# Optimization experiments

Measured on AMD Instinct MI355X. Metric: run time of the kernel, lower is better.

## Reference

```python
import jax, jax.numpy as jnp
import numpy as np

V_IPC, N_ROLES, D = 50000, 16, 256
B, L = 2048, 64
F_BIB, H1, H2, D_OUT = 512, 1024, 1024, 512
N_EXP, N_CLS = 8, 10
LN_EPS = 1e-5


def setup_inputs() -> dict:
    key = jax.random.key(0)
    ks = jax.random.split(key, 24)
    s = 0.05
    ipc_emb = jax.random.normal(ks[0], (V_IPC, D), jnp.float32) * s
    ipc_emb = ipc_emb.at[0].set(0.0)  # padding_idx=0
    role_emb = jax.random.normal(ks[1], (N_ROLES, D), jnp.float32) * s
    role_emb = role_emb.at[0].set(0.0)
    inp = {
        "ipc_indices": jax.random.randint(ks[2], (B, L), 0, V_IPC),
        "role_indices": jax.random.randint(ks[3], (B, L), 0, N_ROLES),
        "bibliometric_features": jax.random.normal(ks[4], (B, F_BIB), jnp.float32),
        "ipc_padding_mask": jax.random.randint(ks[5], (B, L), 0, 2).astype(jnp.int32),
        "top_k": 2,
        "ipc_emb": ipc_emb,
        "role_emb": role_emb,
        "Wq": jax.random.normal(ks[6], (D, D), jnp.float32) * s,
        "bq": jnp.zeros((D,), jnp.float32),
        "Wk": jax.random.normal(ks[7], (D, D), jnp.float32) * s,
        "bk": jnp.zeros((D,), jnp.float32),
        "Wv": jax.random.normal(ks[8], (D, D), jnp.float32) * s,
        "bv": jnp.zeros((D,), jnp.float32),
        "global_context": jax.random.normal(ks[9], (D,), jnp.float32) * s,
        "ln_g": jnp.ones((D,), jnp.float32),
        "ln_b": jnp.zeros((D,), jnp.float32),
        "gate_W": jax.random.normal(ks[10], (D, N_EXP), jnp.float32) * s,
        "gate_b": jnp.zeros((N_EXP,), jnp.float32),
        "expert_biases": jnp.zeros((N_EXP,), jnp.float32),
        "W1": jax.random.normal(ks[11], (N_EXP, F_BIB, H1), jnp.float32) * s,
        "b1": jnp.zeros((N_EXP, H1), jnp.float32),
        "W2": jax.random.normal(ks[12], (N_EXP, H1, H2), jnp.float32) * s,
        "b2": jnp.zeros((N_EXP, H2), jnp.float32),
        "W3": jax.random.normal(ks[13], (N_EXP, H2, D_OUT), jnp.float32) * s,
        "b3": jnp.zeros((N_EXP, D_OUT), jnp.float32),
        "head_W": jax.random.normal(ks[14], (D_OUT, N_CLS), jnp.float32) * s,
        "head_b": jnp.zeros((N_CLS,), jnp.float32),
    }
    return inp


def reference(ipc_indices, role_indices, bibliometric_features, ipc_padding_mask, top_k,
              ipc_emb, role_emb, Wq, bq, Wk, bk, Wv, bv, global_context, ln_g, ln_b,
              gate_W, gate_b, expert_biases, W1, b1, W2, b2, W3, b3, head_W, head_b):
    # embeddings + role combine  -> [B, L, D]
    x = ipc_emb[ipc_indices] + role_emb[role_indices]
    # attention pooling with a global learned query (same query for every batch row)
    keys = x @ Wk + bk                                  # [B, L, D]
    values = x @ Wv + bv                                # [B, L, D]
    q = global_context @ Wq + bq                        # [D]
    scores = jnp.einsum('d,bld->bl', q, keys)           # [B, L]
    scores = jnp.where(ipc_padding_mask == 0, -1e9, scores)
    attn = jax.nn.softmax(scores, axis=-1)              # [B, L]
    pooled = jnp.einsum('bl,bld->bd', attn, values)     # [B, D]
    mu = pooled.mean(-1, keepdims=True)
    var = ((pooled - mu) ** 2).mean(-1, keepdims=True)
    router_in = (pooled - mu) / jnp.sqrt(var + LN_EPS) * ln_g + ln_b
    # router: select with biased scores, gate with unbiased scores
    affinity = router_in @ gate_W + gate_b              # [B, E]
    sel_scores = affinity + expert_biases
    _, idx = jax.lax.top_k(sel_scores, top_k)           # [B, K]
    gw = jax.nn.softmax(jnp.take_along_axis(affinity, idx, axis=-1), axis=-1)  # [B, K]
    # dense all-expert MLP (reference form of masked per-expert loop)
    h = jax.nn.relu(jnp.einsum('bi,eih->ebh', bibliometric_features, W1) + b1[:, None, :])
    h = jax.nn.relu(jnp.einsum('ebh,ehj->ebj', h, W2) + b2[:, None, :])
    eo = jnp.einsum('ebj,ejo->ebo', h, W3) + b3[:, None, :]  # [E, B, O]
    # gather each token's top-k expert outputs and combine
    bidx = jnp.arange(idx.shape[0])[:, None]            # [B, 1]
    sel_out = eo[idx, bidx]                             # [B, K, O]
    moe_out = jnp.einsum('bk,bko->bo', gw, sel_out)     # [B, O]
    logits = moe_out @ head_W + head_b                  # [B, n_classes]
    return logits, idx
```

## Files before the change

kernel.cpp:

```cpp
#include <hip/hip_runtime.h>
#include <hip/hip_bf16.h>
#include <math.h>


#define LN_EPS 1e-5f

typedef __bf16 bf16_t;
typedef __bf16 bf16x8 __attribute__((ext_vector_type(8)));
typedef float f32x4 __attribute__((ext_vector_type(4)));

struct f4x2 { float4 a, b; };
__device__ __forceinline__ f4x2 ldA8(const float* p) {
  f4x2 v; v.a = *(const float4*)p; v.b = *(const float4*)(p + 4); return v;
}
__device__ __forceinline__ bf16x8 cvt8(const f4x2& v) {
  bf16x8 o;
  o[0] = (bf16_t)v.a.x; o[1] = (bf16_t)v.a.y; o[2] = (bf16_t)v.a.z; o[3] = (bf16_t)v.a.w;
  o[4] = (bf16_t)v.b.x; o[5] = (bf16_t)v.b.y; o[6] = (bf16_t)v.b.z; o[7] = (bf16_t)v.b.w;
  return o;
}

__global__ __launch_bounds__(256)
void prep_kq_kernel(const float* __restrict__ Wq, const float* __restrict__ bq,
                    const float* __restrict__ Wk, const float* __restrict__ bk,
                    const float* __restrict__ gc, float* __restrict__ kq_out,
                    int* __restrict__ done_ctr) {
  __shared__ float q[256];
  __shared__ float red[4];
  const int t = threadIdx.x, bi = blockIdx.x;
  if (bi == 0 && t == 0) *done_ctr = 0;
  float s = bq[t];
  for (int d = 0; d < 256; d++) s += gc[d] * Wq[d * 256 + t];
  q[t] = s;
  __syncthreads();
  const int rl = t >> 5, sl = t & 31;
  const int r = bi * 8 + rl;
  float p = 0.f;
#pragma unroll
  for (int i = 0; i < 8; i++) { const int d = sl + 32 * i; p += Wk[r * 256 + d] * q[d]; }
#pragma unroll
  for (int o = 16; o > 0; o >>= 1) p += __shfl_down(p, o, 32);
  if (sl == 0) kq_out[r] = p;
  if (bi == 0) {
    float z2 = q[t] * bk[t];
    const int lane = t & 63, wave = t >> 6;
#pragma unroll
    for (int o = 32; o > 0; o >>= 1) z2 += __shfl_down(z2, o);
    if (lane == 0) red[wave] = z2;
    __syncthreads();
    if (t == 0) kq_out[256] = red[0] + red[1] + red[2] + red[3];
  }
}

__global__ __launch_bounds__(256)
void xbar_transpose(const float* __restrict__ W1, const float* __restrict__ W2,
                    const float* __restrict__ W3, bf16_t* __restrict__ B1,
                    bf16_t* __restrict__ B2, bf16_t* __restrict__ B3h,
                    float* __restrict__ b3h_g,
                    const float* __restrict__ b3, const float* __restrict__ head_W,
                    const int* __restrict__ ipc_idx, const int* __restrict__ role_idx,
                    const int* __restrict__ maskp,
                    const float* __restrict__ ipc_emb, const float* __restrict__ role_emb,
                    const float* __restrict__ kq_qbk, float* __restrict__ xbar_g) {
  __shared__ __align__(16) float smem[4480];
  const int bid = blockIdx.x;
  const int t = threadIdx.x, lane = t & 63;

  if (bid < 2048) {
    const int b = bid, wave = t >> 6;
    float* sred = smem;
    float* scores_s = smem + 4352;
    float* attn_s = smem + 4416;
    const float4 kq = *(const float4*)(kq_qbk + lane * 4);
    const float qbk = kq_qbk[256];
    const int rbase = b * 64 + wave * 16;
    int4 m4[4], i4[4], r4[4];
#pragma unroll
    for (int j = 0; j < 4; j++) {
      m4[j] = *(const int4*)(maskp + rbase + j * 4);
      i4[j] = *(const int4*)(ipc_idx + rbase + j * 4);
      r4[j] = *(const int4*)(role_idx + rbase + j * 4);
    }
#pragma unroll
    for (int i = 0; i < 16; i++) {
      const int mki = (&m4[i / 4].x)[i % 4];
      const int ii = mki ? (&i4[i / 4].x)[i % 4] : 0;
      const int ri = mki ? (&r4[i / 4].x)[i % 4] : 0;
      const float4 xe = *(const float4*)(ipc_emb + (size_t)ii * 256 + lane * 4);
      const float4 re = *(const float4*)(role_emb + (size_t)ri * 256 + lane * 4);
      sred[(wave * 64 + lane) * 17 + i] =
          (xe.x + re.x) * kq.x + (xe.y + re.y) * kq.y +
          (xe.z + re.z) * kq.z + (xe.w + re.w) * kq.w;
    }
    __syncthreads();
    {
      const int i_r = lane & 15, g = lane >> 4;
      float s = 0.f;
#pragma unroll
      for (int j = 0; j < 16; j++) s += sred[(wave * 64 + g * 16 + j) * 17 + i_r];
      s += __shfl_xor(s, 16);
      s += __shfl_xor(s, 32);
      const int mval = (&m4[i_r / 4].x)[i_r % 4];
      if (lane < 16) scores_s[wave * 16 + lane] = mval ? (s + qbk) : -1e9f;
    }
    __syncthreads();
    if (wave == 0) {
      const float sv = scores_s[lane];
      float m = sv;
#pragma unroll
      for (int o = 32; o > 0; o >>= 1) m = fmaxf(m, __shfl_xor(m, o));
      const float ev = expf(sv - m);
      float sum = ev;
#pragma unroll
      for (int o = 32; o > 0; o >>= 1) sum += __shfl_xor(sum, o);
      attn_s[lane] = ev / sum;
    }
    __syncthreads();
    float p0 = 0.f, p1 = 0.f, p2 = 0.f, p3 = 0.f;
#pragma unroll
    for (int i = 0; i < 16; i++) {
      const int mki = (&m4[i / 4].x)[i % 4];
      const int ii = mki ? (&i4[i / 4].x)[i % 4] : 0;
      const int ri = mki ? (&r4[i / 4].x)[i % 4] : 0;
      const float a = attn_s[wave * 16 + i];
      const float4 xe = *(const float4*)(ipc_emb + (size_t)ii * 256 + lane * 4);
      const float4 re = *(const float4*)(role_emb + (size_t)ri * 256 + lane * 4);
      p0 += a * (xe.x + re.x); p1 += a * (xe.y + re.y);
      p2 += a * (xe.z + re.z); p3 += a * (xe.w + re.w);
    }
    __syncthreads();
    *(float4*)&smem[wave * 256 + lane * 4] = make_float4(p0, p1, p2, p3);
    __syncthreads();
    xbar_g[(size_t)b * 256 + t] = smem[t] + smem[256 + t] + smem[512 + t] + smem[768 + t];
    return;
  }

  const int bid2 = bid - 2048;
  if (bid2 >= 3072) {
    const int q = bid2 - 3072;
    const int e = q >> 5, kt = q & 31;
    const int wave = t >> 6;
    float* w3h_s = smem;
    for (int i = t; i < 32 * 16; i += 256) w3h_s[i] = 0.f;
    __syncthreads();
    const int ob = lane * 8;
#pragma unroll
    for (int r = 0; r < 8; r++) {
      const int kl = wave * 8 + r;
      const int k = kt * 32 + kl;
      const f4x2 wv = ldA8(W3 + ((size_t)e * 1024 + k) * 512 + ob);
      for (int c = 0; c < 10; c++) {
        float p = wv.a.x * head_W[(ob + 0) * 10 + c] + wv.a.y * head_W[(ob + 1) * 10 + c] +
                  wv.a.z * head_W[(ob + 2) * 10 + c] + wv.a.w * head_W[(ob + 3) * 10 + c] +
                  wv.b.x * head_W[(ob + 4) * 10 + c] + wv.b.y * head_W[(ob + 5) * 10 + c] +
                  wv.b.z * head_W[(ob + 6) * 10 + c] + wv.b.w * head_W[(ob + 7) * 10 + c];
#pragma unroll
        for (int o = 32; o > 0; o >>= 1) p += __shfl_down(p, o);
        if (lane == 0) w3h_s[kl * 16 + c] = p;
      }
    }
    __syncthreads();
    if (wave == 0) {
      bf16x8 o8;
      const int n_l = lane & 15, k_l = (lane >> 4) * 8;
#pragma unroll
      for (int j = 0; j < 8; j++) o8[j] = (bf16_t)w3h_s[(k_l + j) * 16 + n_l];
      *(bf16x8*)(B3h + (size_t)e * 16 * 1024 + ((size_t)kt * 64 + lane) * 8) = o8;
    }
    if (kt == 0 && wave == 1) {
      for (int c = 0; c < 10; c++) {
        float p = 0.f;
#pragma unroll
        for (int j = 0; j < 8; j++) p += b3[e * 512 + ob + j] * head_W[(ob + j) * 10 + c];
#pragma unroll
        for (int o = 32; o > 0; o >>= 1) p += __shfl_down(p, o);
        if (lane == 0) b3h_g[e * 16 + c] = p;
      }
      if (lane >= 10 && lane < 16) b3h_g[e * 16 + lane] = 0.f;
    }
    return;
  }

  const float* W; bf16_t* Bft; int K, N, e, n0, k0;
  if (bid2 < 1024) {
    W = W1; Bft = B1; K = 512; N = 1024;
    e = bid2 >> 7; const int r = bid2 & 127;
    n0 = (r & 15) * 64; k0 = (r >> 4) * 64;
  } else {
    W = W2; Bft = B2; K = 1024; N = 1024;
    const int q = bid2 - 1024; e = q >> 8; const int r = q & 255;
    n0 = (r & 15) * 64; k0 = (r >> 4) * 64;
  }
  float (*tile)[65] = (float(*)[65])smem;
  const float* Wp = W + (size_t)e * K * N;
  bf16_t* Bp = Bft + (size_t)e * N * K;
  const int tq = t & 15, th = t >> 4;
#pragma unroll
  for (int i = 0; i < 4; i++) {
    const int row = th + 16 * i;
    *(float4*)&tile[row][tq * 4] = *(const float4*)(Wp + (size_t)(k0 + row) * N + n0 + tq * 4);
  }
  __syncthreads();
  const int sub = t >> 6;
  const int nk = K >> 5;
#pragma unroll
  for (int it = 0; it < 2; it++) {
    const int fid = sub + it * 4;
    const int ntl = fid & 3, ktl = fid >> 2;
    const int n_l = ntl * 16 + (lane & 15);
    const int k_l = ktl * 32 + (lane >> 4) * 8;
    bf16x8 o;
#pragma unroll
    for (int j = 0; j < 8; j++) o[j] = (bf16_t)tile[k_l + j][n_l];
    const size_t idx = ((((size_t)(n0 >> 4) + ntl) * nk + (k0 >> 5) + ktl) * 64 + lane) * 8;
    *(bf16x8*)(Bp + idx) = o;
  }
}

__global__ __launch_bounds__(256)
void pool_kernel(const float* __restrict__ xbar_g, const float* __restrict__ Wv,
                 const float* __restrict__ bvec,
                 const float* __restrict__ ln_g, const float* __restrict__ ln_b,
                 const float* __restrict__ gate_W, const float* __restrict__ gate_b,
                 const float* __restrict__ expert_biases,
                 float* __restrict__ out_idx_f, int* __restrict__ ws_idx,
                 float* __restrict__ ws_gw, int* __restrict__ done_ctr,
                 int* __restrict__ list_token, int* __restrict__ a_of,
                 int* __restrict__ offsets_g) {
  const int rb = blockIdx.x * 8;
  __shared__ __align__(16) float xs[8][256];
  __shared__ __align__(16) float pp[4][8][256];
  __shared__ int is_last;
  const int t = threadIdx.x, wave = t >> 6, lane = t & 63;
  for (int i = t; i < 512; i += 256)
    ((float4*)xs)[i] = ((const float4*)(xbar_g + (size_t)rb * 256))[i];
  __syncthreads();
  f32x4 acc[8];
#pragma unroll
  for (int r = 0; r < 8; r++) acc[r] = (f32x4){0.f, 0.f, 0.f, 0.f};
  const int dbase = wave * 64;
  for (int dd = 0; dd < 64; dd += 4) {
    float4 xr[8];
#pragma unroll
    for (int r = 0; r < 8; r++) xr[r] = *(const float4*)&xs[r][dbase + dd];
#pragma unroll
    for (int j = 0; j < 4; j++) {
      const float4 wv = *(const float4*)(Wv + (size_t)(dbase + dd + j) * 256 + lane * 4);
#pragma unroll
      for (int r = 0; r < 8; r++) {
        const float xv = (&xr[r].x)[j];
        acc[r][0] += xv * wv.x; acc[r][1] += xv * wv.y;
        acc[r][2] += xv * wv.z; acc[r][3] += xv * wv.w;
      }
    }
  }
#pragma unroll
  for (int r = 0; r < 8; r++) *(f32x4*)&pp[wave][r][lane * 4] = acc[r];
  __syncthreads();
  const float4 bvv = *(const float4*)(bvec + lane * 4);
  const float4 lg = *(const float4*)(ln_g + lane * 4);
  const float4 lb = *(const float4*)(ln_b + lane * 4);
#pragma unroll
  for (int rr = 0; rr < 2; rr++) {
    const int r = wave * 2 + rr;
    f32x4 v = *(const f32x4*)&pp[0][r][lane * 4];
#pragma unroll
    for (int w2 = 1; w2 < 4; w2++) {
      const f32x4 qv = *(const f32x4*)&pp[w2][r][lane * 4];
      v[0] += qv[0]; v[1] += qv[1]; v[2] += qv[2]; v[3] += qv[3];
    }
    v[0] += bvv.x; v[1] += bvv.y; v[2] += bvv.z; v[3] += bvv.w;
    float s1 = v[0] + v[1] + v[2] + v[3];
#pragma unroll
    for (int o = 32; o > 0; o >>= 1) s1 += __shfl_xor(s1, o);
    const float mu = s1 * (1.f / 256.f);
    const float4 df = make_float4(v[0] - mu, v[1] - mu, v[2] - mu, v[3] - mu);
    float s2 = df.x * df.x + df.y * df.y + df.z * df.z + df.w * df.w;
#pragma unroll
    for (int o = 32; o > 0; o >>= 1) s2 += __shfl_xor(s2, o);
    const float inv = 1.f / sqrtf(s2 * (1.f / 256.f) + LN_EPS);
    f32x4 rv;
    rv[0] = df.x * inv * lg.x + lb.x; rv[1] = df.y * inv * lg.y + lb.y;
    rv[2] = df.z * inv * lg.z + lb.z; rv[3] = df.w * inv * lg.w + lb.w;
    f32x4 pa = {0.f, 0.f, 0.f, 0.f}, pb = {0.f, 0.f, 0.f, 0.f};
#pragma unroll
    for (int k = 0; k < 4; k++) {
      const int d = lane * 4 + k;
      const f32x4 g0 = *(const f32x4*)(gate_W + d * 8);
      const f32x4 g1 = *(const f32x4*)(gate_W + d * 8 + 4);
      pa += rv[k] * g0;
      pb += rv[k] * g1;
    }
#pragma unroll
    for (int o = 32; o > 0; o >>= 1) {
      pa[0] += __shfl_down(pa[0], o); pa[1] += __shfl_down(pa[1], o);
      pa[2] += __shfl_down(pa[2], o); pa[3] += __shfl_down(pa[3], o);
      pb[0] += __shfl_down(pb[0], o); pb[1] += __shfl_down(pb[1], o);
      pb[2] += __shfl_down(pb[2], o); pb[3] += __shfl_down(pb[3], o);
    }
    if (lane == 0) {
      float aff[8];
#pragma unroll
      for (int j = 0; j < 4; j++) { aff[j] = pa[j] + gate_b[j]; aff[4 + j] = pb[j] + gate_b[4 + j]; }
      float b0 = -1e30f; int i0 = 0;
#pragma unroll
      for (int j = 0; j < 8; j++) {
        const float s = aff[j] + expert_biases[j];
        if (s > b0) { b0 = s; i0 = j; }
      }
      float b1v = -1e30f; int i1 = 0;
#pragma unroll
      for (int j = 0; j < 8; j++) {
        const float s = aff[j] + expert_biases[j];
        if (j != i0 && s > b1v) { b1v = s; i1 = j; }
      }
      const float a0 = aff[i0], a1 = aff[i1];
      const float m = fmaxf(a0, a1);
      const float e0 = expf(a0 - m), e1 = expf(a1 - m);
      const float invs = 1.f / (e0 + e1);
      const int bg = rb + r;
      ws_idx[bg * 2] = i0; ws_idx[bg * 2 + 1] = i1;
      ws_gw[bg * 2] = e0 * invs; ws_gw[bg * 2 + 1] = e1 * invs;
      out_idx_f[bg * 2] = (float)i0; out_idx_f[bg * 2 + 1] = (float)i1;
    }
  }
  __syncthreads();
  if (t == 0) {
    __threadfence();
    const int prev = atomicAdd(done_ctr, 1);
    is_last = (prev == (int)gridDim.x - 1);
  }
  __syncthreads();
  if (is_last) {
    __threadfence();
    __shared__ int cnt[8]; __shared__ int offp[9]; __shared__ int fill[8];
    if (t < 8) cnt[t] = 0;
    __syncthreads();
    for (int a = t; a < 4096; a += 256) atomicAdd(&cnt[ws_idx[a]], 1);
    __syncthreads();
    if (t == 0) {
      offp[0] = 0;
      for (int e = 0; e < 8; e++) offp[e + 1] = offp[e] + ((cnt[e] + 63) & ~63);
    }
    __syncthreads();
    if (t < 8) fill[t] = offp[t];
    if (t < 9) offsets_g[t] = offp[t];
    for (int a = t; a < 4608; a += 256) list_token[a] = 0;
    __syncthreads();
    for (int a = t; a < 4096; a += 256) {
      const int e = ws_idx[a];
      const int pos = atomicAdd(&fill[e], 1);
      list_token[pos] = a >> 1;
      a_of[a] = pos;
    }
  }
}

template <int NT, bool RELU>
__global__ __launch_bounds__(256)
void expert_gemm_g1(const float* __restrict__ bib, const int* __restrict__ list_token,
                    const bf16_t* __restrict__ Bft, const float* __restrict__ bias,
                    bf16_t* __restrict__ C, const int* __restrict__ offsets) {
  constexpr int K = 512, nk = K / 32;
  const int e = blockIdx.z;
  const int seg_hi = offsets[e + 1];
  const int blk_row = offsets[e] + blockIdx.y * 128;
  if (blk_row >= seg_hi) return;
  const int wave = threadIdx.x >> 6, lane = threadIdx.x & 63;
  const int row0 = blk_row + wave * 32;
  if (row0 >= seg_hi) return;
  const int n0 = blockIdx.x * 64;
  const int tok0 = list_token[row0 + (lane & 15)];
  const int tok1 = list_token[row0 + 16 + (lane & 15)];
  const float* Ap0 = bib + (size_t)tok0 * 512 + (lane >> 4) * 8;
  const float* Ap1 = bib + (size_t)tok1 * 512 + (lane >> 4) * 8;
  const bf16_t* Bp = Bft + (size_t)e * NT * K + ((size_t)(n0 >> 4) * nk * 512 + lane * 8);
  f32x4 acc[2][4];
#pragma unroll
  for (int i = 0; i < 2; i++)
#pragma unroll
    for (int j = 0; j < 4; j++) acc[i][j] = (f32x4){0.f, 0.f, 0.f, 0.f};
  f4x2 aS[2][2]; bf16x8 bX[2][4];
  aS[0][0] = ldA8(Ap0); aS[0][1] = ldA8(Ap1);
#pragma unroll
  for (int ni = 0; ni < 4; ni++) bX[0][ni] = *(const bf16x8*)(Bp + (size_t)ni * nk * 512);
#pragma unroll
  for (int kt = 0; kt < nk; kt++) {
    const int cur = kt & 1, nxt = cur ^ 1;
    if (kt + 1 < nk) {
      aS[nxt][0] = ldA8(Ap0 + (kt + 1) * 32);
      aS[nxt][1] = ldA8(Ap1 + (kt + 1) * 32);
#pragma unroll
      for (int ni = 0; ni < 4; ni++)
        bX[nxt][ni] = *(const bf16x8*)(Bp + ((size_t)ni * nk + kt + 1) * 512);
    }
    const bf16x8 a0 = cvt8(aS[cur][0]), a1 = cvt8(aS[cur][1]);
#pragma unroll
    for (int ni = 0; ni < 4; ni++) {
      acc[0][ni] = __builtin_amdgcn_mfma_f32_16x16x32_bf16(a0, bX[cur][ni], acc[0][ni], 0, 0, 0);
      acc[1][ni] = __builtin_amdgcn_mfma_f32_16x16x32_bf16(a1, bX[cur][ni], acc[1][ni], 0, 0, 0);
    }
  }
  const int fr = lane & 15, q = lane >> 4;
#pragma unroll
  for (int ni = 0; ni < 4; ni++) {
    const int col = n0 + ni * 16 + fr;
    const float bv = bias[e * NT + col];
#pragma unroll
    for (int mi = 0; mi < 2; mi++) {
#pragma unroll
      for (int r = 0; r < 4; r++) {
        const int row = row0 + mi * 16 + q * 4 + r;
        float v = acc[mi][ni][r] + bv;
        if (RELU) v = fmaxf(v, 0.f);
        C[(size_t)row * NT + col] = (bf16_t)v;
      }
    }
  }
}

template <int K, int NT, int NFRAG, bool RELU, typename OUT_T>
__global__ __launch_bounds__(256)
void expert_gemm_ft(const bf16_t* __restrict__ A, const bf16_t* __restrict__ Bft,
                    const float* __restrict__ bias, OUT_T* __restrict__ C,
                    const int* __restrict__ offsets) {
  constexpr int nk = K / 32;
  const int e = blockIdx.z;
  const int seg_hi = offsets[e + 1];
  const int blk_row = offsets[e] + blockIdx.y * 128;
  if (blk_row >= seg_hi) return;
  const int wave = threadIdx.x >> 6, lane = threadIdx.x & 63;
  const int row0 = blk_row + wave * 32;
  if (row0 >= seg_hi) return;
  const int n0 = blockIdx.x * (16 * NFRAG);
  const bf16_t* Ap = A + (size_t)(row0 + (lane & 15)) * K + ((lane >> 4) * 8);
  const bf16_t* Bp = Bft + (size_t)e * NT * K + ((size_t)(n0 >> 4) * nk * 512 + lane * 8);
  f32x4 acc[2][NFRAG];
#pragma unroll
  for (int i = 0; i < 2; i++)
#pragma unroll
    for (int j = 0; j < NFRAG; j++) acc[i][j] = (f32x4){0.f, 0.f, 0.f, 0.f};
  bf16x8 aX[2][2], bX[2][NFRAG];
#pragma unroll
  for (int mi = 0; mi < 2; mi++) aX[0][mi] = *(const bf16x8*)(Ap + mi * 16 * K);
#pragma unroll
  for (int ni = 0; ni < NFRAG; ni++) bX[0][ni] = *(const bf16x8*)(Bp + (size_t)ni * nk * 512);
#pragma unroll
  for (int kt = 0; kt < nk; kt++) {
    const int cur = kt & 1, nxt = cur ^ 1;
    if (kt + 1 < nk) {
#pragma unroll
      for (int mi = 0; mi < 2; mi++)
        aX[nxt][mi] = *(const bf16x8*)(Ap + mi * 16 * K + (kt + 1) * 32);
#pragma unroll
      for (int ni = 0; ni < NFRAG; ni++)
        bX[nxt][ni] = *(const bf16x8*)(Bp + ((size_t)ni * nk + kt + 1) * 512);
    }
#pragma unroll
    for (int mi = 0; mi < 2; mi++)
#pragma unroll
      for (int ni = 0; ni < NFRAG; ni++)
        acc[mi][ni] = __builtin_amdgcn_mfma_f32_16x16x32_bf16(aX[cur][mi], bX[cur][ni], acc[mi][ni], 0, 0, 0);
  }
  const int fr = lane & 15, q = lane >> 4;
#pragma unroll
  for (int ni = 0; ni < NFRAG; ni++) {
    const int col = n0 + ni * 16 + fr;
    const float bv = bias[e * NT + col];
#pragma unroll
    for (int mi = 0; mi < 2; mi++) {
#pragma unroll
      for (int r = 0; r < 4; r++) {
        const int row = row0 + mi * 16 + q * 4 + r;
        float v = acc[mi][ni][r] + bv;
        if (RELU) v = fmaxf(v, 0.f);
        C[(size_t)row * NT + col] = (OUT_T)v;
      }
    }
  }
}

__global__ __launch_bounds__(256)
void head_small(const float* __restrict__ OcH, const int* __restrict__ a_of,
                const float* __restrict__ ws_gw, const float* __restrict__ head_b,
                float* __restrict__ out) {
  const int tid = blockIdx.x * 256 + threadIdx.x;
  if (tid >= 20480) return;
  const int b = tid / 10, c = tid - b * 10;
  const int a0 = a_of[b * 2], a1 = a_of[b * 2 + 1];
  const float g0 = ws_gw[b * 2], g1 = ws_gw[b * 2 + 1];
  out[tid] = g0 * OcH[(size_t)a0 * 16 + c] + g1 * OcH[(size_t)a1 * 16 + c] + head_b[c];
}

extern "C" void kernel_launch(void* const* d_in, const int* in_sizes, int n_in,
                              void* d_out, int out_size, void* d_ws, size_t ws_size,
                              hipStream_t stream) {
  const int* ipc_idx = (const int*)d_in[0];
  const int* role_idx = (const int*)d_in[1];
  const float* bib = (const float*)d_in[2];
  const int* maskp = (const int*)d_in[3];
  const float* ipc_emb = (const float*)d_in[5];
  const float* role_emb = (const float*)d_in[6];
  const float* Wq = (const float*)d_in[7];
  const float* bq = (const float*)d_in[8];
  const float* Wk = (const float*)d_in[9];
  const float* bk = (const float*)d_in[10];
  const float* Wv = (const float*)d_in[11];
  const float* bv = (const float*)d_in[12];
  const float* gc = (const float*)d_in[13];
  const float* ln_g = (const float*)d_in[14];
  const float* ln_b = (const float*)d_in[15];
  const float* gate_W = (const float*)d_in[16];
  const float* gate_b = (const float*)d_in[17];
  const float* exp_b = (const float*)d_in[18];
  const float* W1 = (const float*)d_in[19];
  const float* b1 = (const float*)d_in[20];
  const float* W2 = (const float*)d_in[21];
  const float* b2 = (const float*)d_in[22];
  const float* W3 = (const float*)d_in[23];
  const float* b3 = (const float*)d_in[24];
  const float* head_W = (const float*)d_in[25];
  const float* head_b = (const float*)d_in[26];

  char* ws = (char*)d_ws;
  size_t off = 0;
  auto alloc = [&](size_t bytes) -> char* {
    char* p = ws + off;
    off += (bytes + 255) & ~(size_t)255;
    return p;
  };
  float* kq_qbk = (float*)alloc(257 * 4);
  float* xbar_g = (float*)alloc((size_t)2048 * 256 * 4);
  int* ws_idx = (int*)alloc(4096 * 4);
  float* ws_gw = (float*)alloc(4096 * 4);
  int* list_tok = (int*)alloc(4608 * 4);
  int* a_of = (int*)alloc(4096 * 4);
  int* offs = (int*)alloc(9 * 4);
  int* done_ctr = (int*)alloc(4);
  float* b3h = (float*)alloc(8 * 16 * 4);
  bf16_t* W1t = (bf16_t*)alloc((size_t)8 * 1024 * 512 * 2);
  bf16_t* W2t = (bf16_t*)alloc((size_t)8 * 1024 * 1024 * 2);
  bf16_t* B3h = (bf16_t*)alloc((size_t)8 * 16 * 1024 * 2);
  bf16_t* H1c = (bf16_t*)alloc((size_t)4608 * 1024 * 2);
  bf16_t* H2c = (bf16_t*)alloc((size_t)4608 * 1024 * 2);
  float* OcH = (float*)alloc((size_t)4608 * 16 * 4);
  (void)in_sizes; (void)n_in; (void)out_size; (void)ws_size;

  float* out_logits = (float*)d_out;
  float* out_idx = (float*)d_out + 20480;

  prep_kq_kernel<<<32, 256, 0, stream>>>(Wq, bq, Wk, bk, gc, kq_qbk, done_ctr);
  xbar_transpose<<<5376, 256, 0, stream>>>(W1, W2, W3, W1t, W2t, B3h, b3h,
                                           b3, head_W,
                                           ipc_idx, role_idx, maskp,
                                           ipc_emb, role_emb, kq_qbk, xbar_g);
  pool_kernel<<<256, 256, 0, stream>>>(xbar_g, Wv, bv, ln_g, ln_b, gate_W, gate_b,
                                       exp_b, out_idx, ws_idx, ws_gw,
                                       done_ctr, list_tok, a_of, offs);
  expert_gemm_g1<1024, true><<<dim3(16, 36, 8), 256, 0, stream>>>(bib, list_tok, W1t, b1, H1c, offs);
  expert_gemm_ft<1024, 1024, 4, true, bf16_t><<<dim3(16, 36, 8), 256, 0, stream>>>(H1c, W2t, b2, H2c, offs);
  expert_gemm_ft<1024, 16, 1, false, float><<<dim3(1, 36, 8), 256, 0, stream>>>(H2c, B3h, b3h, OcH, offs);
  head_small<<<80, 256, 0, stream>>>(OcH, a_of, ws_gw, head_b, out_logits);
}
```

Before: 381.6 us.

## Compute W3·head_W fold with bf16 MFMA and move head prep to prep kernel

The per-expert product of W3 and head_W was computed with scalar FMAs and 10 wave shuffle-reductions per row across 256 blocks. It now runs as bf16 MFMA 16x16x32 tiles over 64 blocks, reading a padded, pre-transposed bf16 copy of head_W. That copy and the b3·head_W bias fold are built in spare waves of prep_kq_kernel. The fold gets cheaper and the grid shrinks, at the cost of rounding W3 to bf16 before the head product and scattered scalar bf16 stores.

```diff
diff --git a/kernel.cpp b/kernel.cpp
--- a/kernel.cpp
+++ b/kernel.cpp
@@ -24,10 +24,13 @@
 void prep_kq_kernel(const float* __restrict__ Wq, const float* __restrict__ bq,
                     const float* __restrict__ Wk, const float* __restrict__ bk,
                     const float* __restrict__ gc, float* __restrict__ kq_out,
-                    int* __restrict__ done_ctr) {
+                    int* __restrict__ done_ctr,
+                    const float* __restrict__ head_W, const float* __restrict__ b3,
+                    bf16_t* __restrict__ hwft, float* __restrict__ b3h_g) {
   __shared__ float q[256];
   __shared__ float red[4];
   const int t = threadIdx.x, bi = blockIdx.x;
+  const int lane = t & 63, wave = t >> 6;
   if (bi == 0 && t == 0) *done_ctr = 0;
   float s = bq[t];
   for (int d = 0; d < 256; d++) s += gc[d] * Wq[d * 256 + t];
@@ -43,12 +46,44 @@
   if (sl == 0) kq_out[r] = p;
   if (bi == 0) {
     float z2 = q[t] * bk[t];
-    const int lane = t & 63, wave = t >> 6;
 #pragma unroll
     for (int o = 32; o > 0; o >>= 1) z2 += __shfl_down(z2, o);
     if (lane == 0) red[wave] = z2;
     __syncthreads();
     if (t == 0) kq_out[256] = red[0] + red[1] + red[2] + red[3];
+  }
+  if (bi < 16 && wave == 1) {
+    bf16x8 o8;
+    const int c = lane & 15, koff = (lane >> 4) * 8;
+#pragma unroll
+    for (int j = 0; j < 8; j++) {
+      const int k = bi * 32 + koff + j;
+      o8[j] = (c < 10) ? (bf16_t)head_W[k * 10 + c] : (bf16_t)0.f;
+    }
+    *(bf16x8*)(hwft + ((size_t)bi * 64 + lane) * 8) = o8;
+  }
+  if (bi >= 16 && bi < 24 && wave == 2) {
+    const int e = bi - 16;
+    float pc[10];
+#pragma unroll
+    for (int c = 0; c < 10; c++) pc[c] = 0.f;
+    for (int jj = 0; jj < 8; jj++) {
+      const int j = lane + jj * 64;
+      const float bv = b3[e * 512 + j];
+#pragma unroll
+      for (int c = 0; c < 10; c++) pc[c] += bv * head_W[j * 10 + c];
+    }
+#pragma unroll
+    for (int c = 0; c < 10; c++) {
+#pragma unroll
+      for (int o = 32; o > 0; o >>= 1) pc[c] += __shfl_down(pc[c], o);
+    }
+    if (lane == 0) {
+#pragma unroll
+      for (int c = 0; c < 10; c++) b3h_g[e * 16 + c] = pc[c];
+#pragma unroll
+      for (int c = 10; c < 16; c++) b3h_g[e * 16 + c] = 0.f;
+    }
   }
 }
 
@@ -56,8 +91,7 @@
 void xbar_transpose(const float* __restrict__ W1, const float* __restrict__ W2,
                     const float* __restrict__ W3, bf16_t* __restrict__ B1,
                     bf16_t* __restrict__ B2, bf16_t* __restrict__ B3h,
-                    float* __restrict__ b3h_g,
-                    const float* __restrict__ b3, const float* __restrict__ head_W,
+                    const bf16_t* __restrict__ hwft,
                     const int* __restrict__ ipc_idx, const int* __restrict__ role_idx,
                     const int* __restrict__ maskp,
                     const float* __restrict__ ipc_emb, const float* __restrict__ role_emb,
@@ -138,45 +172,34 @@
   const int bid2 = bid - 2048;
   if (bid2 >= 3072) {
     const int q = bid2 - 3072;
-    const int e = q >> 5, kt = q & 31;
+    const int e = q >> 3, chunk = q & 7;
     const int wave = t >> 6;
-    float* w3h_s = smem;
-    for (int i = t; i < 32 * 16; i += 256) w3h_s[i] = 0.f;
-    __syncthreads();
-    const int ob = lane * 8;
-#pragma unroll
-    for (int r = 0; r < 8; r++) {
-      const int kl = wave * 8 + r;
-      const int k = kt * 32 + kl;
-      const f4x2 wv = ldA8(W3 + ((size_t)e * 1024 + k) * 512 + ob);
-      for (int c = 0; c < 10; c++) {
-        float p = wv.a.x * head_W[(ob + 0) * 10 + c] + wv.a.y * head_W[(ob + 1) * 10 + c] +
-                  wv.a.z * head_W[(ob + 2) * 10 + c] + wv.a.w * head_W[(ob + 3) * 10 + c] +
-                  wv.b.x * head_W[(ob + 4) * 10 + c] + wv.b.y * head_W[(ob + 5) * 10 + c] +
-                  wv.b.z * head_W[(ob + 6) * 10 + c] + wv.b.w * head_W[(ob + 7) * 10 + c];
-#pragma unroll
-        for (int o = 32; o > 0; o >>= 1) p += __shfl_down(p, o);
-        if (lane == 0) w3h_s[kl * 16 + c] = p;
+    const int row0 = chunk * 128 + wave * 32;
+    const float* Ap0 = W3 + ((size_t)e * 1024 + row0 + (lane & 15)) * 512 + (lane >> 4) * 8;
+    const float* Ap1 = Ap0 + (size_t)16 * 512;
+    const bf16_t* Bp = hwft + lane * 8;
+    f32x4 acc[2];
+    acc[0] = (f32x4){0.f, 0.f, 0.f, 0.f};
+    acc[1] = (f32x4){0.f, 0.f, 0.f, 0.f};
+#pragma unroll
+    for (int kt = 0; kt < 16; kt++) {
+      const bf16x8 a0 = cvt8(ldA8(Ap0 + kt * 32));
+      const bf16x8 a1 = cvt8(ldA8(Ap1 + kt * 32));
+      const bf16x8 bfr = *(const bf16x8*)(Bp + kt * 512);
+      acc[0] = __builtin_amdgcn_mfma_f32_16x16x32_bf16(a0, bfr, acc[0], 0, 0, 0);
+      acc[1] = __builtin_amdgcn_mfma_f32_16x16x32_bf16(a1, bfr, acc[1], 0, 0, 0);
+    }
+    const int col = lane & 15, qq = lane >> 4;
+#pragma unroll
+    for (int mi = 0; mi < 2; mi++) {
+#pragma unroll
+      for (int r2 = 0; r2 < 4; r2++) {
+        const int krow = row0 + mi * 16 + qq * 4 + r2;
+        const int ktp = krow >> 5;
+        const int lanep = col | (((krow >> 3) & 3) << 4);
+        const int jp = krow & 7;
+        B3h[(size_t)e * 16 * 1024 + ((size_t)ktp * 64 + lanep) * 8 + jp] = (bf16_t)acc[mi][r2];
       }
-    }
-    __syncthreads();
-    if (wave == 0) {
-      bf16x8 o8;
-      const int n_l = lane & 15, k_l = (lane >> 4) * 8;
-#pragma unroll
-      for (int j = 0; j < 8; j++) o8[j] = (bf16_t)w3h_s[(k_l + j) * 16 + n_l];
-      *(bf16x8*)(B3h + (size_t)e * 16 * 1024 + ((size_t)kt * 64 + lane) * 8) = o8;
-    }
-    if (kt == 0 && wave == 1) {
-      for (int c = 0; c < 10; c++) {
-        float p = 0.f;
-#pragma unroll
-        for (int j = 0; j < 8; j++) p += b3[e * 512 + ob + j] * head_W[(ob + j) * 10 + c];
-#pragma unroll
-        for (int o = 32; o > 0; o >>= 1) p += __shfl_down(p, o);
-        if (lane == 0) b3h_g[e * 16 + c] = p;
-      }
-      if (lane >= 10 && lane < 16) b3h_g[e * 16 + lane] = 0.f;
     }
     return;
   }
@@ -538,6 +561,7 @@
   int* offs = (int*)alloc(9 * 4);
   int* done_ctr = (int*)alloc(4);
   float* b3h = (float*)alloc(8 * 16 * 4);
+  bf16_t* hwft = (bf16_t*)alloc((size_t)16 * 64 * 8 * 2);
   bf16_t* W1t = (bf16_t*)alloc((size_t)8 * 1024 * 512 * 2);
   bf16_t* W2t = (bf16_t*)alloc((size_t)8 * 1024 * 1024 * 2);
   bf16_t* B3h = (bf16_t*)alloc((size_t)8 * 16 * 1024 * 2);
@@ -549,9 +573,9 @@
   float* out_logits = (float*)d_out;
   float* out_idx = (float*)d_out + 20480;
 
-  prep_kq_kernel<<<32, 256, 0, stream>>>(Wq, bq, Wk, bk, gc, kq_qbk, done_ctr);
-  xbar_transpose<<<5376, 256, 0, stream>>>(W1, W2, W3, W1t, W2t, B3h, b3h,
-                                           b3, head_W,
+  prep_kq_kernel<<<32, 256, 0, stream>>>(Wq, bq, Wk, bk, gc, kq_qbk, done_ctr,
+                                         head_W, b3, hwft, b3h);
+  xbar_transpose<<<5184, 256, 0, stream>>>(W1, W2, W3, W1t, W2t, B3h, hwft,
                                            ipc_idx, role_idx, maskp,
                                            ipc_emb, role_emb, kq_qbk, xbar_g);
   pool_kernel<<<256, 256, 0, stream>>>(xbar_g, Wv, bv, ln_g, ln_b, gate_W, gate_b,
```

Result: faster. 350.9 us (-8.0%).
